# Optimization experiments

Hardware: AMD Instinct MI355X
Metric: run time of the kernel (lower is better)

Reference implementation:

```python
import jax, jax.numpy as jnp
import numpy as np

BIN_SIZE = 500      # bin_size from __init__
K = 5               # num_neighbors
DIST_MULT = 0.1
MAX_NUM_BINS = 200


def setup_inputs() -> dict:
    key = jax.random.key(0)
    k1, k2 = jax.random.split(key)
    points = jax.random.normal(k1, (2, 5000, 64), dtype=jnp.float32)
    # codebook_random_rotations: [n_features, max_num_bins // 2]
    rotations = jax.random.normal(k2, (64, MAX_NUM_BINS // 2), dtype=jnp.float32)
    return {"points": points, "rotations": rotations}


def reference(points, rotations):
    """Dense equivalent of the batched tf.SparseTensor output [B, N, N].

    tf.sparse.add sums duplicate (src, dst) entries, which scatter-add
    reproduces exactly.
    """
    B, N, F = points.shape
    nbins = N // BIN_SIZE

    # LSH projection: use first nbins//2 rotation columns, mirror with -mul.
    mul = jnp.einsum('bnf,fh->bnh', points, rotations[:, : nbins // 2])
    cmul = jnp.concatenate([mul, -mul], axis=-1)          # [B, N, nbins]
    bin_idx = jnp.argmax(cmul, axis=-1)                   # [B, N]
    # split_indices_to_bins: stable argsort of bin assignment, reshape to bins
    bins_split = jnp.argsort(bin_idx, axis=-1, stable=True).reshape(B, nbins, BIN_SIZE)

    # gather points into bins: [B, nbins, BIN_SIZE, F]
    parts = jnp.take_along_axis(points, bins_split.reshape(B, N, 1), axis=1)
    parts = parts.reshape(B, nbins, BIN_SIZE, F)

    # pairwise_dist within each bin
    na = jnp.sum(parts * parts, axis=-1)                  # [B, nbins, bs]
    gram = jnp.einsum('bgif,bgjf->bgij', parts, parts)    # [B, nbins, bs, bs]
    dm = jnp.sqrt(jnp.maximum(na[..., :, None] - 2.0 * gram + na[..., None, :], 1e-6))
    aff = jnp.exp(-DIST_MULT * dm)                        # [B, nbins, bs, bs]

    # top-k neighbors per point within its bin
    vals, idx = jax.lax.top_k(aff, K)                     # [B, nbins, bs, K]

    # map local bin indices back to global point indices
    dst = jax.vmap(jax.vmap(lambda b, i: b[i]))(bins_split, idx)   # [B, nbins, bs, K]
    src = jnp.broadcast_to(bins_split[..., None], dst.shape)
    b_ix = jnp.broadcast_to(jnp.arange(B)[:, None, None, None], dst.shape)

    # scatter-add (duplicates summed, as in repeated tf.sparse.add)
    out = jnp.zeros((B, N, N), dtype=points.dtype)
    out = out.at[b_ix, src, dst].add(vals)
    return out
```

## Files before the change

### kernel.cpp

```cpp
#include <hip/hip_runtime.h>
#include <cfloat>
#include <cstddef>

#define NBATCH 2
#define NPTS   5000
#define NF     64
#define NB     10
#define BINSZ  500
#define TOPK   5
#define ROTCOLS 100

__global__ __launch_bounds__(256) void bin_norm_k(const float* __restrict__ pts,
                                                  const float* __restrict__ rot,
                                                  int* __restrict__ bin_idx,
                                                  float* __restrict__ na) {
    int pt   = blockIdx.x * 4 + (threadIdx.x >> 6);
    int lane = threadIdx.x & 63;
    float p  = pts[(size_t)pt * NF + lane];
    float nn = p * p;
    float c0 = p * rot[lane * ROTCOLS + 0];
    float c1 = p * rot[lane * ROTCOLS + 1];
    float c2 = p * rot[lane * ROTCOLS + 2];
    float c3 = p * rot[lane * ROTCOLS + 3];
    float c4 = p * rot[lane * ROTCOLS + 4];
    #pragma unroll
    for (int off = 32; off > 0; off >>= 1) {
        nn += __shfl_xor(nn, off);
        c0 += __shfl_xor(c0, off);
        c1 += __shfl_xor(c1, off);
        c2 += __shfl_xor(c2, off);
        c3 += __shfl_xor(c3, off);
        c4 += __shfl_xor(c4, off);
    }
    if (lane == 0) {
        float c[5] = {c0, c1, c2, c3, c4};
        float bv = c[0]; int bi = 0;
        #pragma unroll
        for (int h = 1; h < 5; ++h) if (c[h] > bv) { bv = c[h]; bi = h; }
        #pragma unroll
        for (int h = 0; h < 5; ++h) if (-c[h] > bv) { bv = -c[h]; bi = h + 5; }
        bin_idx[pt] = bi;
        na[pt] = nn;
    }
}

__global__ __launch_bounds__(256) void sort_k(const int* __restrict__ bin_idx,
                                              int* __restrict__ order) {
    const int b = blockIdx.x;
    const int t = threadIdx.x;
    __shared__ int sh_bin[NPTS];
    __shared__ int sh_hist[256][NB];
    __shared__ int sh_start[NB + 1];
    for (int i = t; i < NPTS; i += 256) sh_bin[i] = bin_idx[b * NPTS + i];
    #pragma unroll
    for (int h = 0; h < NB; ++h) sh_hist[t][h] = 0;
    __syncthreads();
    const int CH = (NPTS + 255) / 256;
    const int i0 = t * CH;
    const int i1 = (i0 + CH < NPTS) ? (i0 + CH) : NPTS;
    for (int i = i0; i < i1; ++i) sh_hist[t][sh_bin[i]]++;
    __syncthreads();
    if (t < NB) {
        int tot = 0;
        for (int c = 0; c < 256; ++c) tot += sh_hist[c][t];
        sh_start[t + 1] = tot;
    }
    __syncthreads();
    if (t == 0) {
        sh_start[0] = 0;
        for (int h = 1; h <= NB; ++h) sh_start[h] += sh_start[h - 1];
    }
    __syncthreads();
    if (t < NB) {
        int run = sh_start[t];
        for (int c = 0; c < 256; ++c) { int v = sh_hist[c][t]; sh_hist[c][t] = run; run += v; }
    }
    __syncthreads();
    for (int i = i0; i < i1; ++i) {
        int h = sh_bin[i];
        order[b * NPTS + sh_hist[t][h]++] = i;
    }
}

__global__ __launch_bounds__(256) void pair_topk_k(const float* __restrict__ pts,
                                                   const float* __restrict__ na,
                                                   const int* __restrict__ order,
                                                   float* __restrict__ out) {
    const int bx  = blockIdx.x;
    const int g   = bx >> 3;
    const int rb  = bx & 7;
    const int b   = g / NB;
    const int grp = g % NB;
    const int r0  = rb * 64;
    const int tid = threadIdx.x;
    const int w   = tid >> 6;
    const int lane = tid & 63;

    __shared__ float sh_pts[BINSZ * NF];
    __shared__ float sh_na[BINSZ];
    __shared__ int   sh_idx[BINSZ];
    __shared__ float sh_mv[4][64][TOPK];
    __shared__ int   sh_mi[4][64][TOPK];

    const int* ord = order + b * NPTS + grp * BINSZ;
    for (int i = tid; i < BINSZ; i += 256) sh_idx[i] = ord[i];
    __syncthreads();

    const float* pbase = pts + (size_t)b * NPTS * NF;
    float4* sp4 = (float4*)sh_pts;
    for (int q = tid; q < BINSZ * (NF / 4); q += 256) {
        int j = q >> 4, f4 = q & 15;
        sp4[q] = ((const float4*)(pbase + (size_t)sh_idx[j] * NF))[f4];
    }
    for (int i = tid; i < BINSZ; i += 256) sh_na[i] = na[b * NPTS + sh_idx[i]];
    __syncthreads();

    const int rr  = r0 + lane;
    const int rcl = (rr < BINSZ) ? rr : (BINSZ - 1);
    float4 rowr[16];
    #pragma unroll
    for (int q = 0; q < 16; ++q) rowr[q] = sp4[rcl * 16 + q];
    const float na_r = sh_na[rcl];

    float tv[TOPK]; int ti[TOPK];
    #pragma unroll
    for (int s = 0; s < TOPK; ++s) { tv[s] = FLT_MAX; ti[s] = 0; }

    const int cbase = w * 125;
    for (int j = cbase; j < cbase + 125; ++j) {
        const float4* cp = sp4 + j * 16;
        float acc = 0.f;
        #pragma unroll
        for (int q = 0; q < 16; ++q) {
            float4 cc = cp[q];
            acc += rowr[q].x * cc.x;
            acc += rowr[q].y * cc.y;
            acc += rowr[q].z * cc.z;
            acc += rowr[q].w * cc.w;
        }
        float d2 = na_r - 2.f * acc + sh_na[j];
        if (d2 < tv[TOPK - 1]) {
            tv[TOPK - 1] = d2; ti[TOPK - 1] = j;
            #pragma unroll
            for (int s = TOPK - 1; s > 0; --s) {
                if (tv[s] < tv[s - 1]) {
                    float fv = tv[s]; tv[s] = tv[s - 1]; tv[s - 1] = fv;
                    int   fi = ti[s]; ti[s] = ti[s - 1]; ti[s - 1] = fi;
                }
            }
        }
    }

    #pragma unroll
    for (int s = 0; s < TOPK; ++s) { sh_mv[w][lane][s] = tv[s]; sh_mi[w][lane][s] = ti[s]; }
    __syncthreads();

    if (tid < 64) {
        const int r = tid;
        if (r0 + r < BINSZ) {
            int h0 = 0, h1 = 0, h2 = 0, h3 = 0;
            const int src = sh_idx[r0 + r];
            float* orow = out + ((size_t)b * NPTS + src) * NPTS;
            #pragma unroll
            for (int s = 0; s < TOPK; ++s) {
                float v0 = sh_mv[0][r][h0];
                float v1 = sh_mv[1][r][h1];
                float v2 = sh_mv[2][r][h2];
                float v3 = sh_mv[3][r][h3];
                float best = v0; int bw = 0;
                if (v1 < best) { best = v1; bw = 1; }
                if (v2 < best) { best = v2; bw = 2; }
                if (v3 < best) { best = v3; bw = 3; }
                int j;
                if      (bw == 0) { j = sh_mi[0][r][h0]; h0++; }
                else if (bw == 1) { j = sh_mi[1][r][h1]; h1++; }
                else if (bw == 2) { j = sh_mi[2][r][h2]; h2++; }
                else              { j = sh_mi[3][r][h3]; h3++; }
                float dm  = sqrtf(fmaxf(best, 1e-6f));
                float val = expf(-0.1f * dm);
                orow[sh_idx[j]] = val;
            }
        }
    }
}

extern "C" void kernel_launch(void* const* d_in, const int* in_sizes, int n_in,
                              void* d_out, int out_size, void* d_ws, size_t ws_size,
                              hipStream_t stream) {
    const float* points = (const float*)d_in[0];
    const float* rot    = (const float*)d_in[1];
    float* out = (float*)d_out;

    int*   bin_idx = (int*)d_ws;
    float* na      = (float*)((char*)d_ws + NBATCH * NPTS * sizeof(int));
    int*   order   = (int*)((char*)d_ws + 2 * NBATCH * NPTS * sizeof(int));

    hipMemsetAsync(d_out, 0, (size_t)out_size * sizeof(float), stream);

    bin_norm_k<<<(NBATCH * NPTS) / 4, 256, 0, stream>>>(points, rot, bin_idx, na);
    sort_k<<<NBATCH, 256, 0, stream>>>(bin_idx, order);
    pair_topk_k<<<NBATCH * NB * 8, 256, 0, stream>>>(points, na, order, out);
}
```

Measured before the change: 114.5 us.

## Fuse output zeroing into pair top-k kernel, interleaved with distance compute

Drops the separate memset of the 200 MB dense output. Each pair_topk block now zeroes the output rows it owns, issuing float4 zero stores interleaved with the distance/top-k loop so the stores overlap with compute. The final scatter writes come after a __syncthreads, so the zeroes are ordered before them within the block. The cost is extra address arithmetic in the inner loop, and total runtime may still be bound by write bandwidth.

```diff
diff --git a/kernel.cpp b/kernel.cpp
--- a/kernel.cpp
+++ b/kernel.cpp
@@ -9,6 +9,7 @@
 #define BINSZ  500
 #define TOPK   5
 #define ROTCOLS 100
+#define ROW4   (NPTS / 4)
 
 __global__ __launch_bounds__(256) void bin_norm_k(const float* __restrict__ pts,
                                                   const float* __restrict__ rot,
@@ -126,8 +127,29 @@
     #pragma unroll
     for (int s = 0; s < TOPK; ++s) { tv[s] = FLT_MAX; ti[s] = 0; }
 
+    const int vr   = (r0 + 64 <= BINSZ) ? 64 : (BINSZ - r0);
+    const int tot4 = vr * ROW4;
+    const int nst  = (tot4 + 255) / 256;
+    const size_t obase = (size_t)b * NPTS * NPTS;
+    const float4 z4 = make_float4(0.f, 0.f, 0.f, 0.f);
+    int st = 0;
+
     const int cbase = w * 125;
-    for (int j = cbase; j < cbase + 125; ++j) {
+    for (int jj = 0; jj < 125; ++jj) {
+        #pragma unroll
+        for (int u = 0; u < 3; ++u) {
+            if (st < nst) {
+                int idx = st * 256 + tid;
+                if (idx < tot4) {
+                    int r = idx / ROW4;
+                    int c = idx - r * ROW4;
+                    int src = sh_idx[r0 + r];
+                    ((float4*)(out + obase + (size_t)src * NPTS))[c] = z4;
+                }
+                ++st;
+            }
+        }
+        const int j = cbase + jj;
         const float4* cp = sp4 + j * 16;
         float acc = 0.f;
         #pragma unroll
@@ -150,6 +172,16 @@
             }
         }
     }
+    while (st < nst) {
+        int idx = st * 256 + tid;
+        if (idx < tot4) {
+            int r = idx / ROW4;
+            int c = idx - r * ROW4;
+            int src = sh_idx[r0 + r];
+            ((float4*)(out + obase + (size_t)src * NPTS))[c] = z4;
+        }
+        ++st;
+    }
 
     #pragma unroll
     for (int s = 0; s < TOPK; ++s) { sh_mv[w][lane][s] = tv[s]; sh_mi[w][lane][s] = ti[s]; }
@@ -160,7 +192,7 @@
         if (r0 + r < BINSZ) {
             int h0 = 0, h1 = 0, h2 = 0, h3 = 0;
             const int src = sh_idx[r0 + r];
-            float* orow = out + ((size_t)b * NPTS + src) * NPTS;
+            float* orow = out + obase + (size_t)src * NPTS;
             #pragma unroll
             for (int s = 0; s < TOPK; ++s) {
                 float v0 = sh_mv[0][r][h0];
@@ -195,8 +227,6 @@
     float* na      = (float*)((char*)d_ws + NBATCH * NPTS * sizeof(int));
     int*   order   = (int*)((char*)d_ws + 2 * NBATCH * NPTS * sizeof(int));
 
-    hipMemsetAsync(d_out, 0, (size_t)out_size * sizeof(float), stream);
-
     bin_norm_k<<<(NBATCH * NPTS) / 4, 256, 0, stream>>>(points, rot, bin_idx, na);
     sort_k<<<NBATCH, 256, 0, stream>>>(bin_idx, order);
     pair_topk_k<<<NBATCH * NB * 8, 256, 0, stream>>>(points, na, order, out);
```

After: 118.1 us. 3.2% more time.

## Fuse output zeroing with sparse top-k scatter and parallelize sort prefix scans

Applied to the files above, without the earlier changes.

Instead of a separate memset of the whole 200MB dense output followed by scattered writes, the top-k kernel now writes compact (value, column) pairs to workspace. A new kernel zeroes each group of rows and then injects the five entries per row. The sort kernel's serial 256-wide prefix scans are replaced with partial sums and a wave-level shuffle scan, and the bin kernel stages its rotation columns in shared memory. The extra kernel adds a launch and workspace traffic, and the zeroing pass remains bandwidth-bound.

```diff
diff --git a/kernel.cpp b/kernel.cpp
--- a/kernel.cpp
+++ b/kernel.cpp
@@ -9,20 +9,29 @@
 #define BINSZ  500
 #define TOPK   5
 #define ROTCOLS 100
+#define ROW4   (NPTS / 4)
 
 __global__ __launch_bounds__(256) void bin_norm_k(const float* __restrict__ pts,
                                                   const float* __restrict__ rot,
                                                   int* __restrict__ bin_idx,
                                                   float* __restrict__ na) {
-    int pt   = blockIdx.x * 4 + (threadIdx.x >> 6);
-    int lane = threadIdx.x & 63;
+    __shared__ float srot[NF * 5];
+    const int t = threadIdx.x;
+    for (int i = t; i < NF * 5; i += 256) {
+        int f = i / 5, h = i - 5 * f;
+        srot[i] = rot[f * ROTCOLS + h];
+    }
+    __syncthreads();
+
+    int pt   = blockIdx.x * 4 + (t >> 6);
+    int lane = t & 63;
     float p  = pts[(size_t)pt * NF + lane];
     float nn = p * p;
-    float c0 = p * rot[lane * ROTCOLS + 0];
-    float c1 = p * rot[lane * ROTCOLS + 1];
-    float c2 = p * rot[lane * ROTCOLS + 2];
-    float c3 = p * rot[lane * ROTCOLS + 3];
-    float c4 = p * rot[lane * ROTCOLS + 4];
+    float c0 = p * srot[lane * 5 + 0];
+    float c1 = p * srot[lane * 5 + 1];
+    float c2 = p * srot[lane * 5 + 2];
+    float c3 = p * srot[lane * 5 + 3];
+    float c4 = p * srot[lane * 5 + 4];
     #pragma unroll
     for (int off = 32; off > 0; off >>= 1) {
         nn += __shfl_xor(nn, off);
@@ -48,34 +57,65 @@
                                               int* __restrict__ order) {
     const int b = blockIdx.x;
     const int t = threadIdx.x;
+    const int w = t >> 6, lane = t & 63;
     __shared__ int sh_bin[NPTS];
     __shared__ int sh_hist[256][NB];
-    __shared__ int sh_start[NB + 1];
+    __shared__ int sh_part[NB][16];
+    __shared__ int sh_tot[NB + 1];
+
     for (int i = t; i < NPTS; i += 256) sh_bin[i] = bin_idx[b * NPTS + i];
     #pragma unroll
     for (int h = 0; h < NB; ++h) sh_hist[t][h] = 0;
     __syncthreads();
+
     const int CH = (NPTS + 255) / 256;
     const int i0 = t * CH;
     const int i1 = (i0 + CH < NPTS) ? (i0 + CH) : NPTS;
     for (int i = i0; i < i1; ++i) sh_hist[t][sh_bin[i]]++;
     __syncthreads();
+
+    if (t < NB * 16) {
+        int h = t >> 4, s = t & 15;
+        int sum = 0;
+        #pragma unroll
+        for (int k = 0; k < 16; ++k) sum += sh_hist[s * 16 + k][h];
+        sh_part[h][s] = sum;
+    }
+    __syncthreads();
     if (t < NB) {
         int tot = 0;
-        for (int c = 0; c < 256; ++c) tot += sh_hist[c][t];
-        sh_start[t + 1] = tot;
+        #pragma unroll
+        for (int s = 0; s < 16; ++s) tot += sh_part[t][s];
+        sh_tot[t + 1] = tot;
     }
     __syncthreads();
     if (t == 0) {
-        sh_start[0] = 0;
-        for (int h = 1; h <= NB; ++h) sh_start[h] += sh_start[h - 1];
-    }
-    __syncthreads();
-    if (t < NB) {
-        int run = sh_start[t];
-        for (int c = 0; c < 256; ++c) { int v = sh_hist[c][t]; sh_hist[c][t] = run; run += v; }
-    }
-    __syncthreads();
+        sh_tot[0] = 0;
+        for (int h = 1; h <= NB; ++h) sh_tot[h] += sh_tot[h - 1];
+    }
+    __syncthreads();
+
+    for (int h = w; h < NB; h += 4) {
+        int base = lane * 4;
+        int v0 = sh_hist[base + 0][h];
+        int v1 = sh_hist[base + 1][h];
+        int v2 = sh_hist[base + 2][h];
+        int v3 = sh_hist[base + 3][h];
+        int lt = v0 + v1 + v2 + v3;
+        int x = lt;
+        #pragma unroll
+        for (int off = 1; off < 64; off <<= 1) {
+            int y = __shfl_up(x, off);
+            if (lane >= off) x += y;
+        }
+        int excl = x - lt + sh_tot[h];
+        sh_hist[base + 0][h] = excl;
+        sh_hist[base + 1][h] = excl + v0;
+        sh_hist[base + 2][h] = excl + v0 + v1;
+        sh_hist[base + 3][h] = excl + v0 + v1 + v2;
+    }
+    __syncthreads();
+
     for (int i = i0; i < i1; ++i) {
         int h = sh_bin[i];
         order[b * NPTS + sh_hist[t][h]++] = i;
@@ -85,7 +125,8 @@
 __global__ __launch_bounds__(256) void pair_topk_k(const float* __restrict__ pts,
                                                    const float* __restrict__ na,
                                                    const int* __restrict__ order,
-                                                   float* __restrict__ out) {
+                                                   float* __restrict__ wv,
+                                                   int* __restrict__ wd) {
     const int bx  = blockIdx.x;
     const int g   = bx >> 3;
     const int rb  = bx & 7;
@@ -127,7 +168,8 @@
     for (int s = 0; s < TOPK; ++s) { tv[s] = FLT_MAX; ti[s] = 0; }
 
     const int cbase = w * 125;
-    for (int j = cbase; j < cbase + 125; ++j) {
+    for (int jj = 0; jj < 125; ++jj) {
+        const int j = cbase + jj;
         const float4* cp = sp4 + j * 16;
         float acc = 0.f;
         #pragma unroll
@@ -160,7 +202,7 @@
         if (r0 + r < BINSZ) {
             int h0 = 0, h1 = 0, h2 = 0, h3 = 0;
             const int src = sh_idx[r0 + r];
-            float* orow = out + ((size_t)b * NPTS + src) * NPTS;
+            const size_t gbase = ((size_t)b * NPTS + src) * TOPK;
             #pragma unroll
             for (int s = 0; s < TOPK; ++s) {
                 float v0 = sh_mv[0][r][h0];
@@ -177,10 +219,26 @@
                 else if (bw == 2) { j = sh_mi[2][r][h2]; h2++; }
                 else              { j = sh_mi[3][r][h3]; h3++; }
                 float dm  = sqrtf(fmaxf(best, 1e-6f));
-                float val = expf(-0.1f * dm);
-                orow[sh_idx[j]] = val;
+                wv[gbase + s] = expf(-0.1f * dm);
+                wd[gbase + s] = sh_idx[j];
             }
         }
+    }
+}
+
+__global__ __launch_bounds__(256) void zero_inject_k(const float* __restrict__ wv,
+                                                     const int* __restrict__ wd,
+                                                     float* __restrict__ out) {
+    const int t = threadIdx.x;
+    const size_t gr0 = (size_t)blockIdx.x * 4;
+    float4* o4 = ((float4*)out) + gr0 * ROW4;
+    const float4 z4 = make_float4(0.f, 0.f, 0.f, 0.f);
+    for (int i = t; i < 4 * ROW4; i += 256) o4[i] = z4;
+    __syncthreads();
+    if (t < 4 * TOPK) {
+        int r = t / TOPK, s = t - r * TOPK;
+        size_t g = gr0 + r;
+        out[g * NPTS + wd[g * TOPK + s]] = wv[g * TOPK + s];
     }
 }
 
@@ -191,13 +249,15 @@
     const float* rot    = (const float*)d_in[1];
     float* out = (float*)d_out;
 
-    int*   bin_idx = (int*)d_ws;
-    float* na      = (float*)((char*)d_ws + NBATCH * NPTS * sizeof(int));
-    int*   order   = (int*)((char*)d_ws + 2 * NBATCH * NPTS * sizeof(int));
-
-    hipMemsetAsync(d_out, 0, (size_t)out_size * sizeof(float), stream);
+    char* ws = (char*)d_ws;
+    int*   bin_idx = (int*)ws;                                   ws += NBATCH * NPTS * sizeof(int);
+    float* na      = (float*)ws;                                 ws += NBATCH * NPTS * sizeof(float);
+    int*   order   = (int*)ws;                                   ws += NBATCH * NPTS * sizeof(int);
+    float* wv      = (float*)ws;                                 ws += NBATCH * NPTS * TOPK * sizeof(float);
+    int*   wd      = (int*)ws;
 
     bin_norm_k<<<(NBATCH * NPTS) / 4, 256, 0, stream>>>(points, rot, bin_idx, na);
     sort_k<<<NBATCH, 256, 0, stream>>>(bin_idx, order);
-    pair_topk_k<<<NBATCH * NB * 8, 256, 0, stream>>>(points, na, order, out);
-}
+    pair_topk_k<<<NBATCH * NB * 8, 256, 0, stream>>>(points, na, order, wv, wd);
+    zero_inject_k<<<(NBATCH * NPTS) / 4, 256, 0, stream>>>(wv, wd, out);
+}
```

Result: no change. 114.2 us (-0.3%).
